# Kernel optimization log

Hardware: AMD Instinct MI355X
Metric: run time of the kernel (lower is better)

The kernel has to match this reference:

```python
import jax, jax.numpy as jnp
import numpy as np
from jax import lax

B, DIM, H, D, P, KER = 256, 1024, 8, 128, 2048, 4  # P = p_factor*DIM, H*D = 1024
HD = H * D

def _lin(key, out_d, in_d):
    return jax.random.normal(key, (out_d, in_d), jnp.float32) * 0.02

def setup_inputs() -> dict:
    key = jax.random.key(0)
    ks = jax.random.split(key, 16)
    return {
        "seq": jax.random.normal(ks[0], (B, DIM), jnp.float32),
        "c_tm1": jnp.zeros((B, H, D, D), jnp.float32),
        "n_tm1": jnp.ones((B, H, D), jnp.float32),
        "m_tm1": jnp.zeros((B, H), jnp.float32),
        "ln_g": jnp.ones((DIM,), jnp.float32), "ln_b": jnp.zeros((DIM,), jnp.float32),
        "Wul": _lin(ks[1], P, DIM), "bul": jnp.zeros((P,), jnp.float32),
        "Wur": _lin(ks[2], HD, DIM), "bur": jnp.zeros((HD,), jnp.float32),
        "conv_w": jax.random.normal(ks[3], (1, 1, KER), jnp.float32) * 0.3,
        "conv_b": jnp.zeros((1,), jnp.float32),
        "Wskip": _lin(ks[4], HD, P),
        "Wi": _lin(ks[5], H, P), "bi": jnp.zeros((H,), jnp.float32),
        "Wf": _lin(ks[6], H, P), "bf": jnp.zeros((H,), jnp.float32),
        "Wo": _lin(ks[7], HD, P), "bo": jnp.zeros((HD,), jnp.float32),
        "Wq": _lin(ks[8], HD, P), "bq": jnp.zeros((HD,), jnp.float32),
        "Wk": _lin(ks[9], HD, P), "bk": jnp.zeros((HD,), jnp.float32),
        "Wv": _lin(ks[10], HD, P), "bv": jnp.zeros((HD,), jnp.float32),
        "gn_g": jnp.ones((HD,), jnp.float32), "gn_b": jnp.zeros((HD,), jnp.float32),
        "Wd": _lin(ks[11], DIM, HD), "bd": jnp.zeros((DIM,), jnp.float32),
    }

def _layernorm(x, g, b, eps=1e-5):
    mu = jnp.mean(x, -1, keepdims=True)
    var = jnp.mean(jnp.square(x - mu), -1, keepdims=True)
    return (x - mu) * lax.rsqrt(var + eps) * g + b

def _groupnorm(x, g, b, h, d, eps=1e-5):
    xh = x.reshape(-1, h, d)
    mu = jnp.mean(xh, -1, keepdims=True)
    var = jnp.mean(jnp.square(xh - mu), -1, keepdims=True)
    xn = (xh - mu) * lax.rsqrt(var + eps)
    return (xn * g.reshape(h, d) + b.reshape(h, d)).reshape(-1, h * d)

def reference(seq, c_tm1, n_tm1, m_tm1, ln_g, ln_b, Wul, bul, Wur, bur, conv_w, conv_b,
              Wskip, Wi, bi, Wf, bf, Wo, bo, Wq, bq, Wk, bk, Wv, bv, gn_g, gn_b, Wd, bd):
    b, h, d = c_tm1.shape[0], c_tm1.shape[1], c_tm1.shape[2]
    ker = conv_w.shape[-1]
    x_n = _layernorm(seq, ln_g, ln_b)
    x_t = x_n @ Wul.T + bul          # [B,P]
    r_t = x_n @ Wur.T + bur          # [B,HD]
    # causal conv along feature axis (Conv1d(1,1,ker) with left pad, trailing pad dropped)
    xp = jnp.pad(x_t[:, None, :], ((0, 0), (0, 0), (ker - 1, 0)))
    x_c = lax.conv_general_dilated(xp, conv_w, (1,), 'VALID')[:, 0, :] + conv_b
    x_c = jax.nn.silu(x_c)           # [B,P]
    q_t = (x_c @ Wq.T + bq).reshape(b, h, d)
    k_t = (x_c @ Wk.T + bk).reshape(b, h, d) / jnp.sqrt(jnp.float32(d))
    v_t = (x_t @ Wv.T + bv).reshape(b, h, d)
    i_t = x_c @ Wi.T + bi            # [B,H]
    f_t = x_c @ Wf.T + bf
    o_t = jax.nn.sigmoid(x_t @ Wo.T + bo)  # [B,HD]
    m_t = jnp.maximum(f_t + m_tm1, i_t)
    i_e = jnp.exp(i_t - m_t)
    f_e = jnp.exp(f_t - m_t + m_tm1)
    c_t = f_e[:, :, None, None] * c_tm1 + i_e[:, :, None, None] * jnp.einsum('bhd,bhp->bhdp', v_t, k_t)
    n_t = f_e[:, :, None] * n_tm1 + i_e[:, :, None] * k_t
    denom = jnp.maximum(jnp.einsum('bhd,bhd->bh', n_t, q_t), 1.0)[:, :, None]
    h_t = o_t * (jnp.einsum('bhdp,bhp->bhd', c_t, q_t) / denom).reshape(b, h * d)
    out = _groupnorm(h_t, gn_g, gn_b, h, d) + x_c @ Wskip.T
    out = out * jax.nn.silu(r_t)
    out = out @ Wd.T + bd
    return out + seq, c_t, n_t, m_t
```

## Files before the change

kernel.cpp:

```cpp
#include <hip/hip_runtime.h>
#include <hip/hip_bf16.h>
#include <math.h>

#define B_   256
#define DIM_ 1024
#define H_   8
#define D_   128
#define P_   2048
#define HD_  1024

typedef short short8 __attribute__((ext_vector_type(8)));
typedef float f32x4 __attribute__((ext_vector_type(4)));

__device__ __forceinline__ float sigf(float x) { return 1.f / (1.f + expf(-x)); }

__device__ __forceinline__ ushort f2bf(float f) {
    return __builtin_bit_cast(unsigned short, __float2bfloat16(f));
}
__device__ __forceinline__ float bf2f(ushort u) {
    unsigned int v = ((unsigned int)u) << 16;
    return __builtin_bit_cast(float, v);
}

#define GLOAD16(gp, lp) \
    __builtin_amdgcn_global_load_lds((const __attribute__((address_space(1))) void*)(gp), \
                                     (__attribute__((address_space(3))) void*)(lp), 16, 0, 0)

#define WOFF_UL    0
#define WOFF_UR    2097152
#define WOFF_Q     3145728
#define WOFF_K     5242880
#define WOFF_SKIP  7340032
#define WOFF_V     9437184
#define WOFF_O     11534336
#define WOFF_D     13631488
#define WOFF_END   14680064

__global__ void wcvt_kernel(const float* __restrict__ s0, const float* __restrict__ s1,
                            const float* __restrict__ s2, const float* __restrict__ s3,
                            const float* __restrict__ s4, const float* __restrict__ s5,
                            const float* __restrict__ s6, const float* __restrict__ s7,
                            ushort* __restrict__ dst) {
    size_t e = ((size_t)blockIdx.x * 256 + threadIdx.x) * 8;
    const float* sp;
    if      (e < WOFF_UR)   { sp = s0 + e; }
    else if (e < WOFF_Q)    { sp = s1 + (e - WOFF_UR); }
    else if (e < WOFF_K)    { sp = s2 + (e - WOFF_Q); }
    else if (e < WOFF_SKIP) { sp = s3 + (e - WOFF_K); }
    else if (e < WOFF_V)    { sp = s4 + (e - WOFF_SKIP); }
    else if (e < WOFF_O)    { sp = s5 + (e - WOFF_V); }
    else if (e < WOFF_D)    { sp = s6 + (e - WOFF_O); }
    else                    { sp = s7 + (e - WOFF_D); }
    f32x4 a = *(const f32x4*)sp;
    f32x4 b = *(const f32x4*)(sp + 4);
    short8 r;
    r[0] = (short)f2bf(a[0]); r[1] = (short)f2bf(a[1]);
    r[2] = (short)f2bf(a[2]); r[3] = (short)f2bf(a[3]);
    r[4] = (short)f2bf(b[0]); r[5] = (short)f2bf(b[1]);
    r[6] = (short)f2bf(b[2]); r[7] = (short)f2bf(b[3]);
    *(short8*)(dst + e) = r;
}

__global__ void ln_kernel(const float* __restrict__ x, const float* __restrict__ g,
                          const float* __restrict__ bt, ushort* __restrict__ y) {
    int b = blockIdx.x, t = threadIdx.x;
    const float* row = x + (size_t)b * DIM_;
    float4 v = *(const float4*)(row + t * 4);
    float s1 = v.x + v.y + v.z + v.w;
    float s2 = v.x * v.x + v.y * v.y + v.z * v.z + v.w * v.w;
    #pragma unroll
    for (int o = 32; o; o >>= 1) { s1 += __shfl_down(s1, o, 64); s2 += __shfl_down(s2, o, 64); }
    __shared__ float r1[4], r2[4];
    __shared__ float mu_s, rs_s;
    int wid = t >> 6, lane = t & 63;
    if (lane == 0) { r1[wid] = s1; r2[wid] = s2; }
    __syncthreads();
    if (t == 0) {
        float S1 = r1[0] + r1[1] + r1[2] + r1[3];
        float S2 = r2[0] + r2[1] + r2[2] + r2[3];
        float mu = S1 / DIM_;
        mu_s = mu;
        rs_s = rsqrtf(S2 / DIM_ - mu * mu + 1e-5f);
    }
    __syncthreads();
    float mu = mu_s, rs = rs_s;
    float4 gg = *(const float4*)(g + t * 4);
    float4 bb = *(const float4*)(bt + t * 4);
    ushort4 o4;
    o4.x = f2bf((v.x - mu) * rs * gg.x + bb.x);
    o4.y = f2bf((v.y - mu) * rs * gg.y + bb.y);
    o4.z = f2bf((v.z - mu) * rs * gg.z + bb.z);
    o4.w = f2bf((v.w - mu) * rs * gg.w + bb.w);
    *(ushort4*)(y + (size_t)b * DIM_ + t * 4) = o4;
}

template <int GID>
__global__ void g_gemm(const ushort* __restrict__ A0, const ushort* __restrict__ A1,
                       const ushort* __restrict__ Wb,
                       const float* __restrict__ b0, const float* __restrict__ b1,
                       const float* __restrict__ b2, const float* __restrict__ b3,
                       const float* __restrict__ b4,
                       float* __restrict__ o0, float* __restrict__ o1, float* __restrict__ o2,
                       float* __restrict__ o3, float* __restrict__ o4v,
                       ushort* __restrict__ aux, const float* __restrict__ seq) {
    constexpr int K = (GID == 1) ? 2048 : 1024;
    constexpr int NT = K / 64;
    const float KSCALE = 0.088388347648318447f;

    __shared__ __align__(16) ushort As[4][64 * 64];
    __shared__ __align__(16) ushort Bs[4][64 * 64];

    int hwid = blockIdx.x;
    int xcd = hwid & 7, q = hwid >> 3;
    int mt = q & 3, g = ((q >> 2) << 3) + xcd;
    int bm = mt << 6, bn = g << 6;

    const ushort* Ab = A0;
    if constexpr (GID == 1) { if (bn >= 3072) Ab = A1; }

    int tid = threadIdx.x;
    int w = tid >> 6, l = tid & 63;
    int wr = w >> 1, wc = w & 1;
    int lr = l & 15, lg = l >> 4;

    int si0 = tid, si1 = 256 + tid;
    int r0 = si0 >> 3, su0 = (si0 & 7) ^ (r0 & 7);
    int r1 = si1 >> 3, su1 = (si1 & 7) ^ (r1 & 7);
    const ushort* gA0 = Ab + (size_t)(bm + r0) * K + su0 * 8;
    const ushort* gA1 = Ab + (size_t)(bm + r1) * K + su1 * 8;
    const ushort* gB0 = Wb + (size_t)(bn + r0) * K + su0 * 8;
    const ushort* gB1 = Wb + (size_t)(bn + r1) * K + su1 * 8;

    f32x4 acc[2][2] = {};

    #pragma unroll
    for (int pt = 0; pt < 2; pt++) {
        int k0 = pt * 64;
        GLOAD16(gA0 + k0, &As[pt][si0 * 8]);
        GLOAD16(gA1 + k0, &As[pt][si1 * 8]);
        GLOAD16(gB0 + k0, &Bs[pt][si0 * 8]);
        GLOAD16(gB1 + k0, &Bs[pt][si1 * 8]);
    }

    for (int t = 0; t < NT; t++) {
        if (t + 2 < NT) {
            int k0 = (t + 2) * 64;
            int nb = (t + 2) & 3;
            GLOAD16(gA0 + k0, &As[nb][si0 * 8]);
            GLOAD16(gA1 + k0, &As[nb][si1 * 8]);
            GLOAD16(gB0 + k0, &Bs[nb][si0 * 8]);
            GLOAD16(gB1 + k0, &Bs[nb][si1 * 8]);
            asm volatile("s_waitcnt vmcnt(8)" ::: "memory");
        } else if (t + 1 < NT) {
            asm volatile("s_waitcnt vmcnt(4)" ::: "memory");
        } else {
            asm volatile("s_waitcnt vmcnt(0)" ::: "memory");
        }
        __builtin_amdgcn_sched_barrier(0);
        __builtin_amdgcn_s_barrier();
        __builtin_amdgcn_sched_barrier(0);

        int cur = t & 3;
        const char* Ac = (const char*)As[cur];
        const char* Bc = (const char*)Bs[cur];
        short8 af[2][2], bf_[2][2];
        #pragma unroll
        for (int mi = 0; mi < 2; mi++) {
            #pragma unroll
            for (int ks = 0; ks < 2; ks++) {
                int r = wr * 32 + mi * 16 + lr;
                int c = (ks * 64 + lg * 16) ^ ((r & 7) << 4);
                af[mi][ks] = *(const short8*)(Ac + r * 128 + c);
            }
        }
        #pragma unroll
        for (int ni = 0; ni < 2; ni++) {
            #pragma unroll
            for (int ks = 0; ks < 2; ks++) {
                int r = wc * 32 + ni * 16 + lr;
                int c = (ks * 64 + lg * 16) ^ ((r & 7) << 4);
                bf_[ni][ks] = *(const short8*)(Bc + r * 128 + c);
            }
        }
        #pragma unroll
        for (int ks = 0; ks < 2; ks++) {
            #pragma unroll
            for (int mi = 0; mi < 2; mi++) {
                #pragma unroll
                for (int ni = 0; ni < 2; ni++) {
                    acc[mi][ni] = __builtin_amdgcn_mfma_f32_16x16x32_bf16(
                        af[mi][ks], bf_[ni][ks], acc[mi][ni], 0, 0, 0);
                }
            }
        }
        __builtin_amdgcn_sched_barrier(0);
    }

    #pragma unroll
    for (int mi = 0; mi < 2; mi++) {
        #pragma unroll
        for (int ni = 0; ni < 2; ni++) {
            int n = bn + wc * 32 + ni * 16 + lr;
            #pragma unroll
            for (int r = 0; r < 4; r++) {
                int m = bm + wr * 32 + mi * 16 + lg * 4 + r;
                float val = acc[mi][ni][r];
                if constexpr (GID == 0) {
                    if (n < 2048) {
                        val += b0[n];
                        o0[(size_t)m * 2048 + n] = val;
                        aux[(size_t)m * 2048 + n] = f2bf(val);
                    } else {
                        int nc = n - 2048;
                        val += b1[nc];
                        o1[(size_t)m * 1024 + nc] = val * sigf(val);
                    }
                } else if constexpr (GID == 1) {
                    if (n < 1024) {
                        o0[(size_t)m * 1024 + n] = val + b0[n];
                    } else if (n < 2048) {
                        int nc = n - 1024;
                        o1[(size_t)m * 1024 + nc] = (val + b1[nc]) * KSCALE;
                    } else if (n < 3072) {
                        int nc = n - 2048;
                        o2[(size_t)m * 1024 + nc] = val;
                    } else if (n < 4096) {
                        int nc = n - 3072;
                        o3[(size_t)m * 1024 + nc] = val + b3[nc];
                    } else {
                        int nc = n - 4096;
                        o4v[(size_t)m * 1024 + nc] = sigf(val + b4[nc]);
                    }
                } else {
                    o0[(size_t)m * 1024 + n] = val + b0[n] + seq[(size_t)m * 1024 + n];
                }
            }
        }
    }
}

__global__ void conv_silu_kernel(const float* __restrict__ x_t, const float* __restrict__ w,
                                 const float* __restrict__ cb, ushort* __restrict__ x_c) {
    int idx = blockIdx.x * 256 + threadIdx.x;
    int b = idx >> 11, p = idx & 2047;
    const float* row = x_t + (size_t)b * P_;
    float acc = cb[0];
    #pragma unroll
    for (int j = 0; j < 4; j++) {
        int pp = p - 3 + j;
        if (pp >= 0) acc = fmaf(w[j], row[pp], acc);
    }
    x_c[idx] = f2bf(acc * (1.f / (1.f + expf(-acc))));
}

__global__ void gates_kernel(const ushort* __restrict__ xc,
                             const float* __restrict__ Wi, const float* __restrict__ Wf,
                             const float* __restrict__ bi, const float* __restrict__ bfp,
                             float* __restrict__ itb, float* __restrict__ ftb) {
    int w = threadIdx.x >> 6, l = threadIdx.x & 63;
    int gid = blockIdx.x * 4 + w;
    int b = gid >> 4, n = gid & 15;
    const float* Wrow = (n < 8) ? (Wi + (size_t)n * 2048) : (Wf + (size_t)(n - 8) * 2048);
    const ushort* arow = xc + (size_t)b * 2048;
    float s = 0.f;
    #pragma unroll
    for (int c = 0; c < 4; c++) {
        int k0 = c * 512 + l * 8;
        short8 a = *(const short8*)(arow + k0);
        f32x4 w0 = *(const f32x4*)(Wrow + k0);
        f32x4 w1 = *(const f32x4*)(Wrow + k0 + 4);
        s = fmaf(bf2f((ushort)a[0]), w0[0], s);
        s = fmaf(bf2f((ushort)a[1]), w0[1], s);
        s = fmaf(bf2f((ushort)a[2]), w0[2], s);
        s = fmaf(bf2f((ushort)a[3]), w0[3], s);
        s = fmaf(bf2f((ushort)a[4]), w1[0], s);
        s = fmaf(bf2f((ushort)a[5]), w1[1], s);
        s = fmaf(bf2f((ushort)a[6]), w1[2], s);
        s = fmaf(bf2f((ushort)a[7]), w1[3], s);
    }
    #pragma unroll
    for (int o = 32; o; o >>= 1) s += __shfl_down(s, o, 64);
    if (l == 0) {
        if (n < 8) itb[b * 8 + n] = s + bi[n];
        else       ftb[b * 8 + (n - 8)] = s + bfp[n - 8];
    }
}

__global__ void cell_kernel(const float* __restrict__ q, const float* __restrict__ k,
                            const float* __restrict__ v, const float* __restrict__ o,
                            const float* __restrict__ i_t, const float* __restrict__ f_t,
                            const float* __restrict__ m_tm1, const float* __restrict__ n_tm1,
                            const float* __restrict__ c_tm1,
                            const float* __restrict__ gn_g, const float* __restrict__ gn_b,
                            const float* __restrict__ skip, const float* __restrict__ sr,
                            float* __restrict__ c_out, float* __restrict__ n_out,
                            float* __restrict__ m_out, ushort* __restrict__ y) {
    int bh = blockIdx.x;
    int h = bh & 7;
    int t = threadIdx.x;
    __shared__ __align__(16) float qs[128];
    __shared__ __align__(16) float ks[128];
    __shared__ __align__(16) float vs[128];
    __shared__ float hnum[128];
    __shared__ float redA[4], redB[4];
    __shared__ float dsh, mu_s, rs_s;

    float fi = i_t[bh], ff = f_t[bh], mo = m_tm1[bh];
    float mt = fmaxf(ff + mo, fi);
    float ie = expf(fi - mt);
    float fe = expf(ff - mt + mo);
    if (t == 0) m_out[bh] = mt;

    int base = bh << 7;
    if (t < 128) { qs[t] = q[base + t]; ks[t] = k[base + t]; vs[t] = v[base + t]; }
    __syncthreads();

    float dn = 0.f;
    if (t < 128) {
        float nt = fe * n_tm1[base + t] + ie * ks[t];
        n_out[base + t] = nt;
        dn = nt * qs[t];
    }
    #pragma unroll
    for (int off2 = 32; off2; off2 >>= 1) dn += __shfl_down(dn, off2, 64);
    int wid = t >> 6, lane = t & 63;
    if (lane == 0) redA[wid] = dn;
    __syncthreads();
    if (t == 0) dsh = fmaxf(redA[0] + redA[1], 1.f);

    const float* cin = c_tm1 + ((size_t)bh << 14);
    float* cout = c_out + ((size_t)bh << 14);
    int l32 = t & 31, grp = t >> 5;
    float4 k4 = *(const float4*)&ks[l32 << 2];
    float4 q4 = *(const float4*)&qs[l32 << 2];
    #pragma unroll
    for (int it2 = 0; it2 < 16; ++it2) {
        int d = (it2 << 3) + grp;
        float vd = vs[d] * ie;
        int off = (d << 7) + (l32 << 2);
        float4 c4 = *(const float4*)(cin + off);
        float4 ct;
        ct.x = fmaf(fe, c4.x, vd * k4.x);
        ct.y = fmaf(fe, c4.y, vd * k4.y);
        ct.z = fmaf(fe, c4.z, vd * k4.z);
        ct.w = fmaf(fe, c4.w, vd * k4.w);
        *(float4*)(cout + off) = ct;
        float p = ct.x * q4.x + ct.y * q4.y + ct.z * q4.z + ct.w * q4.w;
        #pragma unroll
        for (int o2 = 16; o2; o2 >>= 1) p += __shfl_xor(p, o2, 32);
        if (l32 == 0) hnum[d] = p;
    }
    __syncthreads();

    float hval = 0.f;
    if (t < 128) hval = o[base + t] * hnum[t] / dsh;
    float s1 = hval, s2 = hval * hval;
    #pragma unroll
    for (int off2 = 32; off2; off2 >>= 1) { s1 += __shfl_down(s1, off2, 64); s2 += __shfl_down(s2, off2, 64); }
    if (lane == 0) { redA[wid] = s1; redB[wid] = s2; }
    __syncthreads();
    if (t == 0) {
        float S1 = redA[0] + redA[1], S2 = redB[0] + redB[1];
        float mu = S1 / 128.f;
        mu_s = mu;
        rs_s = rsqrtf(S2 / 128.f - mu * mu + 1e-5f);
    }
    __syncthreads();
    if (t < 128) {
        float xn = (hval - mu_s) * rs_s;
        int gi = (h << 7) + t;
        y[base + t] = f2bf((xn * gn_g[gi] + gn_b[gi] + skip[base + t]) * sr[base + t]);
    }
}

extern "C" void kernel_launch(void* const* d_in, const int* in_sizes, int n_in,
                              void* d_out, int out_size, void* d_ws, size_t ws_size,
                              hipStream_t stream) {
    const float* seq    = (const float*)d_in[0];
    const float* c_tm1  = (const float*)d_in[1];
    const float* n_tm1  = (const float*)d_in[2];
    const float* m_tm1  = (const float*)d_in[3];
    const float* ln_g   = (const float*)d_in[4];
    const float* ln_b   = (const float*)d_in[5];
    const float* Wul    = (const float*)d_in[6];
    const float* bul    = (const float*)d_in[7];
    const float* Wur    = (const float*)d_in[8];
    const float* bur    = (const float*)d_in[9];
    const float* conv_w = (const float*)d_in[10];
    const float* conv_b = (const float*)d_in[11];
    const float* Wskip  = (const float*)d_in[12];
    const float* Wi     = (const float*)d_in[13];
    const float* bi     = (const float*)d_in[14];
    const float* Wf     = (const float*)d_in[15];
    const float* bf     = (const float*)d_in[16];
    const float* Wo     = (const float*)d_in[17];
    const float* bo     = (const float*)d_in[18];
    const float* Wq     = (const float*)d_in[19];
    const float* bq     = (const float*)d_in[20];
    const float* Wk     = (const float*)d_in[21];
    const float* bk     = (const float*)d_in[22];
    const float* Wv     = (const float*)d_in[23];
    const float* bv     = (const float*)d_in[24];
    const float* gn_g   = (const float*)d_in[25];
    const float* gn_b   = (const float*)d_in[26];
    const float* Wd     = (const float*)d_in[27];
    const float* bd     = (const float*)d_in[28];

    float* out   = (float*)d_out;
    float* c_out = out + 262144;
    float* n_out = c_out + 33554432;
    float* m_out = n_out + 262144;

    float* ws    = (float*)d_ws;
    float*  x_t  = ws;
    ushort* xnb  = (ushort*)(ws + 524288);
    ushort* xtb  = (ushort*)(ws + 655360);
    float*  sr   = ws + 917504;
    ushort* xcb  = (ushort*)(ws + 1179648);
    float*  qb   = ws + 1441792;
    float*  kb   = ws + 1703936;
    float*  vb   = ws + 1966080;
    float*  ob   = ws + 2228224;
    float*  skipb= ws + 2490368;
    float*  itb  = ws + 2752512;
    float*  ftb  = ws + 2754560;
    ushort* ybf  = (ushort*)(ws + 2756608);
    ushort* wbf  = (ushort*)(ws + 2887680);

    dim3 blk(256);

    wcvt_kernel<<<7168, blk, 0, stream>>>(Wul, Wur, Wq, Wk, Wskip, Wv, Wo, Wd, wbf);
    ln_kernel<<<256, blk, 0, stream>>>(seq, ln_g, ln_b, xnb);
    g_gemm<0><<<192, blk, 0, stream>>>(xnb, nullptr, wbf + WOFF_UL,
                                       bul, bur, nullptr, nullptr, nullptr,
                                       x_t, sr, nullptr, nullptr, nullptr, xtb, nullptr);
    conv_silu_kernel<<<2048, blk, 0, stream>>>(x_t, conv_w, conv_b, xcb);
    gates_kernel<<<1024, blk, 0, stream>>>(xcb, Wi, Wf, bi, bf, itb, ftb);
    g_gemm<1><<<320, blk, 0, stream>>>(xcb, xtb, wbf + WOFF_Q,
                                       bq, bk, nullptr, bv, bo,
                                       qb, kb, skipb, vb, ob, nullptr, nullptr);
    cell_kernel<<<2048, blk, 0, stream>>>(qb, kb, vb, ob, itb, ftb, m_tm1, n_tm1, c_tm1,
                                          gn_g, gn_b, skipb, sr, c_out, n_out, m_out, ybf);
    g_gemm<2><<<64, blk, 0, stream>>>(ybf, nullptr, wbf + WOFF_D,
                                      bd, nullptr, nullptr, nullptr, nullptr,
                                      out, nullptr, nullptr, nullptr, nullptr, nullptr, seq);
}
```

Measured before the change: 388.2 us.

## Fuse layernorm with weight conversion and fold conv and gates into main GEMM

Merges the layernorm and the bf16 weight conversion into one prep kernel. Appends the Wi/Wf gate rows, padded to a tile, to the concatenated weight matrix. The second GEMM now applies the causal conv plus SiLU on the fly from x_t, so the separate conv_silu and gates kernels are gone, along with the xcb buffer and two launches. The trade-off is extra work in the mega GEMM's A-operand path and one additional N-tile column block, 352 blocks instead of 320.

```diff
diff --git a/kernel.cpp b/kernel.cpp
--- a/kernel.cpp
+++ b/kernel.cpp
@@ -2,137 +2,120 @@
 #include <hip/hip_bf16.h>
 #include <math.h>
 
-#define B_   256
-#define DIM_ 1024
-#define H_   8
-#define D_   128
-#define P_   2048
-#define HD_  1024
-
 typedef short short8 __attribute__((ext_vector_type(8)));
 typedef float f32x4 __attribute__((ext_vector_type(4)));
 
 __device__ __forceinline__ float sigf(float x) { return 1.f / (1.f + expf(-x)); }
-
 __device__ __forceinline__ ushort f2bf(float f) {
     return __builtin_bit_cast(unsigned short, __float2bfloat16(f));
 }
-__device__ __forceinline__ float bf2f(ushort u) {
-    unsigned int v = ((unsigned int)u) << 16;
-    return __builtin_bit_cast(float, v);
-}
 
 #define GLOAD16(gp, lp) \
     __builtin_amdgcn_global_load_lds((const __attribute__((address_space(1))) void*)(gp), \
                                      (__attribute__((address_space(3))) void*)(lp), 16, 0, 0)
 
-#define WOFF_UL    0
-#define WOFF_UR    2097152
-#define WOFF_Q     3145728
-#define WOFF_K     5242880
-#define WOFF_SKIP  7340032
-#define WOFF_V     9437184
-#define WOFF_O     11534336
-#define WOFF_D     13631488
-#define WOFF_END   14680064
-
-__global__ void wcvt_kernel(const float* __restrict__ s0, const float* __restrict__ s1,
-                            const float* __restrict__ s2, const float* __restrict__ s3,
-                            const float* __restrict__ s4, const float* __restrict__ s5,
-                            const float* __restrict__ s6, const float* __restrict__ s7,
-                            ushort* __restrict__ dst) {
-    size_t e = ((size_t)blockIdx.x * 256 + threadIdx.x) * 8;
-    const float* sp;
-    if      (e < WOFF_UR)   { sp = s0 + e; }
-    else if (e < WOFF_Q)    { sp = s1 + (e - WOFF_UR); }
-    else if (e < WOFF_K)    { sp = s2 + (e - WOFF_Q); }
-    else if (e < WOFF_SKIP) { sp = s3 + (e - WOFF_K); }
-    else if (e < WOFF_V)    { sp = s4 + (e - WOFF_SKIP); }
-    else if (e < WOFF_O)    { sp = s5 + (e - WOFF_V); }
-    else if (e < WOFF_D)    { sp = s6 + (e - WOFF_O); }
-    else                    { sp = s7 + (e - WOFF_D); }
-    f32x4 a = *(const f32x4*)sp;
-    f32x4 b = *(const f32x4*)(sp + 4);
-    short8 r;
-    r[0] = (short)f2bf(a[0]); r[1] = (short)f2bf(a[1]);
-    r[2] = (short)f2bf(a[2]); r[3] = (short)f2bf(a[3]);
-    r[4] = (short)f2bf(b[0]); r[5] = (short)f2bf(b[1]);
-    r[6] = (short)f2bf(b[2]); r[7] = (short)f2bf(b[3]);
-    *(short8*)(dst + e) = r;
+#define OFF_G0 0
+#define OFF_G1 3145728
+#define OFF_D  14680064
+#define W_END  15728640
+
+__global__ void prep_kernel(const float* __restrict__ seq, const float* __restrict__ ln_g,
+                            const float* __restrict__ ln_b,
+                            const float* __restrict__ Wul, const float* __restrict__ Wur,
+                            const float* __restrict__ Wq, const float* __restrict__ Wk,
+                            const float* __restrict__ Wskip, const float* __restrict__ Wv,
+                            const float* __restrict__ Wo, const float* __restrict__ Wi,
+                            const float* __restrict__ Wf, const float* __restrict__ Wd,
+                            ushort* __restrict__ xnb, ushort* __restrict__ wbf) {
+    int t = threadIdx.x;
+    if (blockIdx.x < 256) {
+        int b = blockIdx.x;
+        const float* row = seq + (size_t)b * 1024;
+        float4 v = *(const float4*)(row + t * 4);
+        float s1 = v.x + v.y + v.z + v.w;
+        float s2 = v.x * v.x + v.y * v.y + v.z * v.z + v.w * v.w;
+        #pragma unroll
+        for (int o = 32; o; o >>= 1) { s1 += __shfl_down(s1, o, 64); s2 += __shfl_down(s2, o, 64); }
+        __shared__ float r1[4], r2[4];
+        __shared__ float mu_s, rs_s;
+        int wid = t >> 6, lane = t & 63;
+        if (lane == 0) { r1[wid] = s1; r2[wid] = s2; }
+        __syncthreads();
+        if (t == 0) {
+            float S1 = r1[0] + r1[1] + r1[2] + r1[3];
+            float S2 = r2[0] + r2[1] + r2[2] + r2[3];
+            float mu = S1 / 1024.f;
+            mu_s = mu;
+            rs_s = rsqrtf(S2 / 1024.f - mu * mu + 1e-5f);
+        }
+        __syncthreads();
+        float mu = mu_s, rs = rs_s;
+        float4 gg = *(const float4*)(ln_g + t * 4);
+        float4 bb = *(const float4*)(ln_b + t * 4);
+        ushort4 o4;
+        o4.x = f2bf((v.x - mu) * rs * gg.x + bb.x);
+        o4.y = f2bf((v.y - mu) * rs * gg.y + bb.y);
+        o4.z = f2bf((v.z - mu) * rs * gg.z + bb.z);
+        o4.w = f2bf((v.w - mu) * rs * gg.w + bb.w);
+        *(ushort4*)(xnb + (size_t)b * 1024 + t * 4) = o4;
+    } else {
+        size_t e = ((size_t)(blockIdx.x - 256) * 256 + t) * 8;
+        const float* sp = nullptr;
+        if (e < OFF_G1) {
+            size_t row = e >> 10, col = e & 1023;
+            sp = (row < 2048 ? Wul + row * 1024 : Wur + (row - 2048) * 1024) + col;
+        } else if (e < OFF_D) {
+            size_t rel = e - OFF_G1;
+            size_t row = rel >> 11, col = rel & 2047;
+            if (row < 1024)      sp = Wq + row * 2048 + col;
+            else if (row < 2048) sp = Wk + (row - 1024) * 2048 + col;
+            else if (row < 3072) sp = Wskip + (row - 2048) * 2048 + col;
+            else if (row < 4096) sp = Wv + (row - 3072) * 2048 + col;
+            else if (row < 5120) sp = Wo + (row - 4096) * 2048 + col;
+            else if (row < 5128) sp = Wi + (row - 5120) * 2048 + col;
+            else if (row < 5136) sp = Wf + (row - 5128) * 2048 + col;
+            else sp = nullptr;
+        } else {
+            sp = Wd + (e - OFF_D);
+        }
+        short8 r;
+        if (sp) {
+            f32x4 a = *(const f32x4*)sp;
+            f32x4 b = *(const f32x4*)(sp + 4);
+            r[0] = (short)f2bf(a[0]); r[1] = (short)f2bf(a[1]);
+            r[2] = (short)f2bf(a[2]); r[3] = (short)f2bf(a[3]);
+            r[4] = (short)f2bf(b[0]); r[5] = (short)f2bf(b[1]);
+            r[6] = (short)f2bf(b[2]); r[7] = (short)f2bf(b[3]);
+        } else {
+            r = (short8){0,0,0,0,0,0,0,0};
+        }
+        *(short8*)(wbf + e) = r;
+    }
 }
 
-__global__ void ln_kernel(const float* __restrict__ x, const float* __restrict__ g,
-                          const float* __restrict__ bt, ushort* __restrict__ y) {
-    int b = blockIdx.x, t = threadIdx.x;
-    const float* row = x + (size_t)b * DIM_;
-    float4 v = *(const float4*)(row + t * 4);
-    float s1 = v.x + v.y + v.z + v.w;
-    float s2 = v.x * v.x + v.y * v.y + v.z * v.z + v.w * v.w;
-    #pragma unroll
-    for (int o = 32; o; o >>= 1) { s1 += __shfl_down(s1, o, 64); s2 += __shfl_down(s2, o, 64); }
-    __shared__ float r1[4], r2[4];
-    __shared__ float mu_s, rs_s;
-    int wid = t >> 6, lane = t & 63;
-    if (lane == 0) { r1[wid] = s1; r2[wid] = s2; }
-    __syncthreads();
-    if (t == 0) {
-        float S1 = r1[0] + r1[1] + r1[2] + r1[3];
-        float S2 = r2[0] + r2[1] + r2[2] + r2[3];
-        float mu = S1 / DIM_;
-        mu_s = mu;
-        rs_s = rsqrtf(S2 / DIM_ - mu * mu + 1e-5f);
-    }
-    __syncthreads();
-    float mu = mu_s, rs = rs_s;
-    float4 gg = *(const float4*)(g + t * 4);
-    float4 bb = *(const float4*)(bt + t * 4);
-    ushort4 o4;
-    o4.x = f2bf((v.x - mu) * rs * gg.x + bb.x);
-    o4.y = f2bf((v.y - mu) * rs * gg.y + bb.y);
-    o4.z = f2bf((v.z - mu) * rs * gg.z + bb.z);
-    o4.w = f2bf((v.w - mu) * rs * gg.w + bb.w);
-    *(ushort4*)(y + (size_t)b * DIM_ + t * 4) = o4;
-}
-
-template <int GID>
-__global__ void g_gemm(const ushort* __restrict__ A0, const ushort* __restrict__ A1,
-                       const ushort* __restrict__ Wb,
-                       const float* __restrict__ b0, const float* __restrict__ b1,
-                       const float* __restrict__ b2, const float* __restrict__ b3,
-                       const float* __restrict__ b4,
-                       float* __restrict__ o0, float* __restrict__ o1, float* __restrict__ o2,
-                       float* __restrict__ o3, float* __restrict__ o4v,
-                       ushort* __restrict__ aux, const float* __restrict__ seq) {
-    constexpr int K = (GID == 1) ? 2048 : 1024;
-    constexpr int NT = K / 64;
-    const float KSCALE = 0.088388347648318447f;
-
-    __shared__ __align__(16) ushort As[4][64 * 64];
-    __shared__ __align__(16) ushort Bs[4][64 * 64];
-
+__global__ void g_gemm0(const ushort* __restrict__ A, const ushort* __restrict__ Wb,
+                        const float* __restrict__ bul, const float* __restrict__ bur,
+                        float* __restrict__ x_t, float* __restrict__ sr,
+                        ushort* __restrict__ xtb) {
+    constexpr int K = 1024, NT = 16;
+    __shared__ __align__(16) ushort As[4][4096];
+    __shared__ __align__(16) ushort Bs[4][4096];
     int hwid = blockIdx.x;
     int xcd = hwid & 7, q = hwid >> 3;
     int mt = q & 3, g = ((q >> 2) << 3) + xcd;
     int bm = mt << 6, bn = g << 6;
-
-    const ushort* Ab = A0;
-    if constexpr (GID == 1) { if (bn >= 3072) Ab = A1; }
-
     int tid = threadIdx.x;
     int w = tid >> 6, l = tid & 63;
     int wr = w >> 1, wc = w & 1;
     int lr = l & 15, lg = l >> 4;
-
     int si0 = tid, si1 = 256 + tid;
     int r0 = si0 >> 3, su0 = (si0 & 7) ^ (r0 & 7);
     int r1 = si1 >> 3, su1 = (si1 & 7) ^ (r1 & 7);
-    const ushort* gA0 = Ab + (size_t)(bm + r0) * K + su0 * 8;
-    const ushort* gA1 = Ab + (size_t)(bm + r1) * K + su1 * 8;
+    const ushort* gA0 = A + (size_t)(bm + r0) * K + su0 * 8;
+    const ushort* gA1 = A + (size_t)(bm + r1) * K + su1 * 8;
     const ushort* gB0 = Wb + (size_t)(bn + r0) * K + su0 * 8;
     const ushort* gB1 = Wb + (size_t)(bn + r1) * K + su1 * 8;
-
     f32x4 acc[2][2] = {};
-
     #pragma unroll
     for (int pt = 0; pt < 2; pt++) {
         int k0 = pt * 64;
@@ -141,11 +124,9 @@
         GLOAD16(gB0 + k0, &Bs[pt][si0 * 8]);
         GLOAD16(gB1 + k0, &Bs[pt][si1 * 8]);
     }
-
     for (int t = 0; t < NT; t++) {
         if (t + 2 < NT) {
-            int k0 = (t + 2) * 64;
-            int nb = (t + 2) & 3;
+            int k0 = (t + 2) * 64, nb = (t + 2) & 3;
             GLOAD16(gA0 + k0, &As[nb][si0 * 8]);
             GLOAD16(gA1 + k0, &As[nb][si1 * 8]);
             GLOAD16(gB0 + k0, &Bs[nb][si0 * 8]);
@@ -159,45 +140,38 @@
         __builtin_amdgcn_sched_barrier(0);
         __builtin_amdgcn_s_barrier();
         __builtin_amdgcn_sched_barrier(0);
-
         int cur = t & 3;
         const char* Ac = (const char*)As[cur];
         const char* Bc = (const char*)Bs[cur];
-        short8 af[2][2], bf_[2][2];
-        #pragma unroll
-        for (int mi = 0; mi < 2; mi++) {
+        short8 af[2][2], bfr[2][2];
+        #pragma unroll
+        for (int mi = 0; mi < 2; mi++)
             #pragma unroll
             for (int ks = 0; ks < 2; ks++) {
                 int r = wr * 32 + mi * 16 + lr;
                 int c = (ks * 64 + lg * 16) ^ ((r & 7) << 4);
                 af[mi][ks] = *(const short8*)(Ac + r * 128 + c);
             }
-        }
-        #pragma unroll
-        for (int ni = 0; ni < 2; ni++) {
+        #pragma unroll
+        for (int ni = 0; ni < 2; ni++)
             #pragma unroll
             for (int ks = 0; ks < 2; ks++) {
                 int r = wc * 32 + ni * 16 + lr;
                 int c = (ks * 64 + lg * 16) ^ ((r & 7) << 4);
-                bf_[ni][ks] = *(const short8*)(Bc + r * 128 + c);
-            }
-        }
-        #pragma unroll
-        for (int ks = 0; ks < 2; ks++) {
-            #pragma unroll
-            for (int mi = 0; mi < 2; mi++) {
-                #pragma unroll
-                for (int ni = 0; ni < 2; ni++) {
+                bfr[ni][ks] = *(const short8*)(Bc + r * 128 + c);
+            }
+        #pragma unroll
+        for (int ks = 0; ks < 2; ks++)
+            #pragma unroll
+            for (int mi = 0; mi < 2; mi++)
+                #pragma unroll
+                for (int ni = 0; ni < 2; ni++)
                     acc[mi][ni] = __builtin_amdgcn_mfma_f32_16x16x32_bf16(
-                        af[mi][ks], bf_[ni][ks], acc[mi][ni], 0, 0, 0);
-                }
-            }
-        }
+                        af[mi][ks], bfr[ni][ks], acc[mi][ni], 0, 0, 0);
         __builtin_amdgcn_sched_barrier(0);
     }
-
-    #pragma unroll
-    for (int mi = 0; mi < 2; mi++) {
+    #pragma unroll
+    for (int mi = 0; mi < 2; mi++)
         #pragma unroll
         for (int ni = 0; ni < 2; ni++) {
             int n = bn + wc * 32 + ni * 16 + lr;
@@ -205,85 +179,224 @@
             for (int r = 0; r < 4; r++) {
                 int m = bm + wr * 32 + mi * 16 + lg * 4 + r;
                 float val = acc[mi][ni][r];
-                if constexpr (GID == 0) {
-                    if (n < 2048) {
-                        val += b0[n];
-                        o0[(size_t)m * 2048 + n] = val;
-                        aux[(size_t)m * 2048 + n] = f2bf(val);
-                    } else {
-                        int nc = n - 2048;
-                        val += b1[nc];
-                        o1[(size_t)m * 1024 + nc] = val * sigf(val);
-                    }
-                } else if constexpr (GID == 1) {
-                    if (n < 1024) {
-                        o0[(size_t)m * 1024 + n] = val + b0[n];
-                    } else if (n < 2048) {
-                        int nc = n - 1024;
-                        o1[(size_t)m * 1024 + nc] = (val + b1[nc]) * KSCALE;
-                    } else if (n < 3072) {
-                        int nc = n - 2048;
-                        o2[(size_t)m * 1024 + nc] = val;
-                    } else if (n < 4096) {
-                        int nc = n - 3072;
-                        o3[(size_t)m * 1024 + nc] = val + b3[nc];
-                    } else {
-                        int nc = n - 4096;
-                        o4v[(size_t)m * 1024 + nc] = sigf(val + b4[nc]);
-                    }
+                if (n < 2048) {
+                    val += bul[n];
+                    x_t[(size_t)m * 2048 + n] = val;
+                    xtb[(size_t)m * 2048 + n] = f2bf(val);
                 } else {
-                    o0[(size_t)m * 1024 + n] = val + b0[n] + seq[(size_t)m * 1024 + n];
+                    int nc = n - 2048;
+                    val += bur[nc];
+                    sr[(size_t)m * 1024 + nc] = val * sigf(val);
                 }
             }
         }
-    }
 }
 
-__global__ void conv_silu_kernel(const float* __restrict__ x_t, const float* __restrict__ w,
-                                 const float* __restrict__ cb, ushort* __restrict__ x_c) {
-    int idx = blockIdx.x * 256 + threadIdx.x;
-    int b = idx >> 11, p = idx & 2047;
-    const float* row = x_t + (size_t)b * P_;
-    float acc = cb[0];
-    #pragma unroll
-    for (int j = 0; j < 4; j++) {
-        int pp = p - 3 + j;
-        if (pp >= 0) acc = fmaf(w[j], row[pp], acc);
-    }
-    x_c[idx] = f2bf(acc * (1.f / (1.f + expf(-acc))));
-}
-
-__global__ void gates_kernel(const ushort* __restrict__ xc,
-                             const float* __restrict__ Wi, const float* __restrict__ Wf,
-                             const float* __restrict__ bi, const float* __restrict__ bfp,
-                             float* __restrict__ itb, float* __restrict__ ftb) {
-    int w = threadIdx.x >> 6, l = threadIdx.x & 63;
-    int gid = blockIdx.x * 4 + w;
-    int b = gid >> 4, n = gid & 15;
-    const float* Wrow = (n < 8) ? (Wi + (size_t)n * 2048) : (Wf + (size_t)(n - 8) * 2048);
-    const ushort* arow = xc + (size_t)b * 2048;
-    float s = 0.f;
-    #pragma unroll
-    for (int c = 0; c < 4; c++) {
-        int k0 = c * 512 + l * 8;
-        short8 a = *(const short8*)(arow + k0);
-        f32x4 w0 = *(const f32x4*)(Wrow + k0);
-        f32x4 w1 = *(const f32x4*)(Wrow + k0 + 4);
-        s = fmaf(bf2f((ushort)a[0]), w0[0], s);
-        s = fmaf(bf2f((ushort)a[1]), w0[1], s);
-        s = fmaf(bf2f((ushort)a[2]), w0[2], s);
-        s = fmaf(bf2f((ushort)a[3]), w0[3], s);
-        s = fmaf(bf2f((ushort)a[4]), w1[0], s);
-        s = fmaf(bf2f((ushort)a[5]), w1[1], s);
-        s = fmaf(bf2f((ushort)a[6]), w1[2], s);
-        s = fmaf(bf2f((ushort)a[7]), w1[3], s);
-    }
-    #pragma unroll
-    for (int o = 32; o; o >>= 1) s += __shfl_down(s, o, 64);
-    if (l == 0) {
-        if (n < 8) itb[b * 8 + n] = s + bi[n];
-        else       ftb[b * 8 + (n - 8)] = s + bfp[n - 8];
-    }
+__global__ void g_mega(const float* __restrict__ xt_f32, const ushort* __restrict__ xtb,
+                       const ushort* __restrict__ Wb,
+                       const float* __restrict__ conv_w, const float* __restrict__ conv_b,
+                       const float* __restrict__ bq, const float* __restrict__ bk,
+                       const float* __restrict__ bv, const float* __restrict__ bo,
+                       const float* __restrict__ bi, const float* __restrict__ bf2,
+                       float* __restrict__ qb, float* __restrict__ kb,
+                       float* __restrict__ skipb, float* __restrict__ vb,
+                       float* __restrict__ ob, float* __restrict__ itb,
+                       float* __restrict__ ftb) {
+    constexpr int K = 2048, NT = 32;
+    const float KSCALE = 0.088388347648318447f;
+    __shared__ __align__(16) ushort As[4][4096];
+    __shared__ __align__(16) ushort Bs[4][4096];
+    int hwid = blockIdx.x;
+    int xcd = hwid & 7, q = hwid >> 3;
+    int mt = q & 3, gq = q >> 2;
+    int g = gq * 8 + xcd;
+    int bm = mt << 6, bn = g << 6;
+    bool is_xc = (bn < 3072) || (bn >= 5120);
+    int tid = threadIdx.x;
+    int w = tid >> 6, l = tid & 63;
+    int wr = w >> 1, wc = w & 1;
+    int lr = l & 15, lg = l >> 4;
+    int si0 = tid, si1 = 256 + tid;
+    int r0 = si0 >> 3, su0 = (si0 & 7) ^ (r0 & 7);
+    int r1 = si1 >> 3, su1 = (si1 & 7) ^ (r1 & 7);
+    const ushort* gB0 = Wb + (size_t)(bn + r0) * K + su0 * 8;
+    const ushort* gB1 = Wb + (size_t)(bn + r1) * K + su1 * 8;
+    f32x4 acc[2][2] = {};
+
+    if (is_xc) {
+        float cw0 = conv_w[0], cw1 = conv_w[1], cw2 = conv_w[2], cw3 = conv_w[3];
+        float cbias = conv_b[0];
+        int ar = tid >> 2, ac4 = tid & 3;
+        const float* arow = xt_f32 + (size_t)(bm + ar) * 2048;
+        int au0 = ((ac4 * 2) ^ (ar & 7)) << 4;
+        int au1 = ((ac4 * 2 + 1) ^ (ar & 7)) << 4;
+        GLOAD16(gB0, &Bs[0][si0 * 8]);
+        GLOAD16(gB1, &Bs[0][si1 * 8]);
+        GLOAD16(gB0 + 64, &Bs[1][si0 * 8]);
+        GLOAD16(gB1 + 64, &Bs[1][si1 * 8]);
+        f32x4 pv0, pv1, pv2, pv3, pv4;
+        {
+            const float* ap = arow + ac4 * 16;
+            if (ac4 == 0) pv0 = (f32x4){0.f, 0.f, 0.f, 0.f};
+            else          pv0 = *(const f32x4*)(ap - 4);
+            pv1 = *(const f32x4*)(ap);
+            pv2 = *(const f32x4*)(ap + 4);
+            pv3 = *(const f32x4*)(ap + 8);
+            pv4 = *(const f32x4*)(ap + 12);
+        }
+        for (int t = 0; t < NT; t++) {
+            f32x4 nv0, nv1, nv2, nv3, nv4;
+            if (t + 1 < NT) {
+                const float* ap = arow + (t + 1) * 64 + ac4 * 16;
+                nv0 = *(const f32x4*)(ap - 4);
+                nv1 = *(const f32x4*)(ap);
+                nv2 = *(const f32x4*)(ap + 4);
+                nv3 = *(const f32x4*)(ap + 8);
+                nv4 = *(const f32x4*)(ap + 12);
+            }
+            if (t + 2 < NT) {
+                int kk = (t + 2) * 64, nb = (t + 2) & 3;
+                GLOAD16(gB0 + kk, &Bs[nb][si0 * 8]);
+                GLOAD16(gB1 + kk, &Bs[nb][si1 * 8]);
+            }
+            float Wv_[20];
+            *(f32x4*)(Wv_ + 0)  = pv0; *(f32x4*)(Wv_ + 4)  = pv1;
+            *(f32x4*)(Wv_ + 8)  = pv2; *(f32x4*)(Wv_ + 12) = pv3;
+            *(f32x4*)(Wv_ + 16) = pv4;
+            short8 p0, p1;
+            #pragma unroll
+            for (int j = 0; j < 16; j++) {
+                float a = fmaf(cw3, Wv_[j + 4], fmaf(cw2, Wv_[j + 3],
+                          fmaf(cw1, Wv_[j + 2], fmaf(cw0, Wv_[j + 1], cbias))));
+                a = a * (1.f / (1.f + expf(-a)));
+                if (j < 8) p0[j] = (short)f2bf(a); else p1[j - 8] = (short)f2bf(a);
+            }
+            char* Aw = (char*)As[t & 1] + ar * 128;
+            *(short8*)(Aw + au0) = p0;
+            *(short8*)(Aw + au1) = p1;
+            asm volatile("s_waitcnt lgkmcnt(0)" ::: "memory");
+            __builtin_amdgcn_sched_barrier(0);
+            __builtin_amdgcn_s_barrier();
+            __builtin_amdgcn_sched_barrier(0);
+            const char* Ac = (const char*)As[t & 1];
+            const char* Bc = (const char*)Bs[t & 3];
+            short8 af[2][2], bfr[2][2];
+            #pragma unroll
+            for (int mi = 0; mi < 2; mi++)
+                #pragma unroll
+                for (int ks = 0; ks < 2; ks++) {
+                    int r = wr * 32 + mi * 16 + lr;
+                    int c = (ks * 64 + lg * 16) ^ ((r & 7) << 4);
+                    af[mi][ks] = *(const short8*)(Ac + r * 128 + c);
+                }
+            #pragma unroll
+            for (int ni = 0; ni < 2; ni++)
+                #pragma unroll
+                for (int ks = 0; ks < 2; ks++) {
+                    int r = wc * 32 + ni * 16 + lr;
+                    int c = (ks * 64 + lg * 16) ^ ((r & 7) << 4);
+                    bfr[ni][ks] = *(const short8*)(Bc + r * 128 + c);
+                }
+            #pragma unroll
+            for (int ks = 0; ks < 2; ks++)
+                #pragma unroll
+                for (int mi = 0; mi < 2; mi++)
+                    #pragma unroll
+                    for (int ni = 0; ni < 2; ni++)
+                        acc[mi][ni] = __builtin_amdgcn_mfma_f32_16x16x32_bf16(
+                            af[mi][ks], bfr[ni][ks], acc[mi][ni], 0, 0, 0);
+            pv0 = nv0; pv1 = nv1; pv2 = nv2; pv3 = nv3; pv4 = nv4;
+            __builtin_amdgcn_sched_barrier(0);
+        }
+    } else {
+        const ushort* gA0 = xtb + (size_t)(bm + r0) * K + su0 * 8;
+        const ushort* gA1 = xtb + (size_t)(bm + r1) * K + su1 * 8;
+        #pragma unroll
+        for (int pt = 0; pt < 2; pt++) {
+            int k0 = pt * 64;
+            GLOAD16(gA0 + k0, &As[pt][si0 * 8]);
+            GLOAD16(gA1 + k0, &As[pt][si1 * 8]);
+            GLOAD16(gB0 + k0, &Bs[pt][si0 * 8]);
+            GLOAD16(gB1 + k0, &Bs[pt][si1 * 8]);
+        }
+        for (int t = 0; t < NT; t++) {
+            if (t + 2 < NT) {
+                int k0 = (t + 2) * 64, nb = (t + 2) & 3;
+                GLOAD16(gA0 + k0, &As[nb][si0 * 8]);
+                GLOAD16(gA1 + k0, &As[nb][si1 * 8]);
+                GLOAD16(gB0 + k0, &Bs[nb][si0 * 8]);
+                GLOAD16(gB1 + k0, &Bs[nb][si1 * 8]);
+                asm volatile("s_waitcnt vmcnt(8)" ::: "memory");
+            } else if (t + 1 < NT) {
+                asm volatile("s_waitcnt vmcnt(4)" ::: "memory");
+            } else {
+                asm volatile("s_waitcnt vmcnt(0)" ::: "memory");
+            }
+            __builtin_amdgcn_sched_barrier(0);
+            __builtin_amdgcn_s_barrier();
+            __builtin_amdgcn_sched_barrier(0);
+            int cur = t & 3;
+            const char* Ac = (const char*)As[cur];
+            const char* Bc = (const char*)Bs[cur];
+            short8 af[2][2], bfr[2][2];
+            #pragma unroll
+            for (int mi = 0; mi < 2; mi++)
+                #pragma unroll
+                for (int ks = 0; ks < 2; ks++) {
+                    int r = wr * 32 + mi * 16 + lr;
+                    int c = (ks * 64 + lg * 16) ^ ((r & 7) << 4);
+                    af[mi][ks] = *(const short8*)(Ac + r * 128 + c);
+                }
+            #pragma unroll
+            for (int ni = 0; ni < 2; ni++)
+                #pragma unroll
+                for (int ks = 0; ks < 2; ks++) {
+                    int r = wc * 32 + ni * 16 + lr;
+                    int c = (ks * 64 + lg * 16) ^ ((r & 7) << 4);
+                    bfr[ni][ks] = *(const short8*)(Bc + r * 128 + c);
+                }
+            #pragma unroll
+            for (int ks = 0; ks < 2; ks++)
+                #pragma unroll
+                for (int mi = 0; mi < 2; mi++)
+                    #pragma unroll
+                    for (int ni = 0; ni < 2; ni++)
+                        acc[mi][ni] = __builtin_amdgcn_mfma_f32_16x16x32_bf16(
+                            af[mi][ks], bfr[ni][ks], acc[mi][ni], 0, 0, 0);
+            __builtin_amdgcn_sched_barrier(0);
+        }
+    }
+
+    int seg = bn >> 10;
+    #pragma unroll
+    for (int mi = 0; mi < 2; mi++)
+        #pragma unroll
+        for (int ni = 0; ni < 2; ni++) {
+            int n = bn + wc * 32 + ni * 16 + lr;
+            #pragma unroll
+            for (int r = 0; r < 4; r++) {
+                int m = bm + wr * 32 + mi * 16 + lg * 4 + r;
+                float val = acc[mi][ni][r];
+                if (seg == 0) {
+                    qb[(size_t)m * 1024 + n] = val + bq[n];
+                } else if (seg == 1) {
+                    int nc = n - 1024;
+                    kb[(size_t)m * 1024 + nc] = (val + bk[nc]) * KSCALE;
+                } else if (seg == 2) {
+                    skipb[(size_t)m * 1024 + (n - 2048)] = val;
+                } else if (seg == 3) {
+                    int nc = n - 3072;
+                    vb[(size_t)m * 1024 + nc] = val + bv[nc];
+                } else if (seg == 4) {
+                    int nc = n - 4096;
+                    ob[(size_t)m * 1024 + nc] = sigf(val + bo[nc]);
+                } else {
+                    int j = n - 5120;
+                    if (j < 8)       itb[m * 8 + j] = val + bi[j];
+                    else if (j < 16) ftb[m * 8 + (j - 8)] = val + bf2[j - 8];
+                }
+            }
+        }
 }
 
 __global__ void cell_kernel(const float* __restrict__ q, const float* __restrict__ k,
@@ -371,6 +484,95 @@
         int gi = (h << 7) + t;
         y[base + t] = f2bf((xn * gn_g[gi] + gn_b[gi] + skip[base + t]) * sr[base + t]);
     }
+}
+
+__global__ void g_gemmD(const ushort* __restrict__ A, const ushort* __restrict__ Wb,
+                        const float* __restrict__ bd, const float* __restrict__ seq,
+                        float* __restrict__ out) {
+    constexpr int K = 1024, NT = 16;
+    __shared__ __align__(16) ushort As[4][4096];
+    __shared__ __align__(16) ushort Bs[4][4096];
+    int hwid = blockIdx.x;
+    int xcd = hwid & 7, q = hwid >> 3;
+    int mt = q & 3, g = ((q >> 2) << 3) + xcd;
+    int bm = mt << 6, bn = g << 6;
+    int tid = threadIdx.x;
+    int w = tid >> 6, l = tid & 63;
+    int wr = w >> 1, wc = w & 1;
+    int lr = l & 15, lg = l >> 4;
+    int si0 = tid, si1 = 256 + tid;
+    int r0 = si0 >> 3, su0 = (si0 & 7) ^ (r0 & 7);
+    int r1 = si1 >> 3, su1 = (si1 & 7) ^ (r1 & 7);
+    const ushort* gA0 = A + (size_t)(bm + r0) * K + su0 * 8;
+    const ushort* gA1 = A + (size_t)(bm + r1) * K + su1 * 8;
+    const ushort* gB0 = Wb + (size_t)(bn + r0) * K + su0 * 8;
+    const ushort* gB1 = Wb + (size_t)(bn + r1) * K + su1 * 8;
+    f32x4 acc[2][2] = {};
+    #pragma unroll
+    for (int pt = 0; pt < 2; pt++) {
+        int k0 = pt * 64;
+        GLOAD16(gA0 + k0, &As[pt][si0 * 8]);
+        GLOAD16(gA1 + k0, &As[pt][si1 * 8]);
+        GLOAD16(gB0 + k0, &Bs[pt][si0 * 8]);
+        GLOAD16(gB1 + k0, &Bs[pt][si1 * 8]);
+    }
+    for (int t = 0; t < NT; t++) {
+        if (t + 2 < NT) {
+            int k0 = (t + 2) * 64, nb = (t + 2) & 3;
+            GLOAD16(gA0 + k0, &As[nb][si0 * 8]);
+            GLOAD16(gA1 + k0, &As[nb][si1 * 8]);
+            GLOAD16(gB0 + k0, &Bs[nb][si0 * 8]);
+            GLOAD16(gB1 + k0, &Bs[nb][si1 * 8]);
+            asm volatile("s_waitcnt vmcnt(8)" ::: "memory");
+        } else if (t + 1 < NT) {
+            asm volatile("s_waitcnt vmcnt(4)" ::: "memory");
+        } else {
+            asm volatile("s_waitcnt vmcnt(0)" ::: "memory");
+        }
+        __builtin_amdgcn_sched_barrier(0);
+        __builtin_amdgcn_s_barrier();
+        __builtin_amdgcn_sched_barrier(0);
+        int cur = t & 3;
+        const char* Ac = (const char*)As[cur];
+        const char* Bc = (const char*)Bs[cur];
+        short8 af[2][2], bfr[2][2];
+        #pragma unroll
+        for (int mi = 0; mi < 2; mi++)
+            #pragma unroll
+            for (int ks = 0; ks < 2; ks++) {
+                int r = wr * 32 + mi * 16 + lr;
+                int c = (ks * 64 + lg * 16) ^ ((r & 7) << 4);
+                af[mi][ks] = *(const short8*)(Ac + r * 128 + c);
+            }
+        #pragma unroll
+        for (int ni = 0; ni < 2; ni++)
+            #pragma unroll
+            for (int ks = 0; ks < 2; ks++) {
+                int r = wc * 32 + ni * 16 + lr;
+                int c = (ks * 64 + lg * 16) ^ ((r & 7) << 4);
+                bfr[ni][ks] = *(const short8*)(Bc + r * 128 + c);
+            }
+        #pragma unroll
+        for (int ks = 0; ks < 2; ks++)
+            #pragma unroll
+            for (int mi = 0; mi < 2; mi++)
+                #pragma unroll
+                for (int ni = 0; ni < 2; ni++)
+                    acc[mi][ni] = __builtin_amdgcn_mfma_f32_16x16x32_bf16(
+                        af[mi][ks], bfr[ni][ks], acc[mi][ni], 0, 0, 0);
+        __builtin_amdgcn_sched_barrier(0);
+    }
+    #pragma unroll
+    for (int mi = 0; mi < 2; mi++)
+        #pragma unroll
+        for (int ni = 0; ni < 2; ni++) {
+            int n = bn + wc * 32 + ni * 16 + lr;
+            #pragma unroll
+            for (int r = 0; r < 4; r++) {
+                int m = bm + wr * 32 + mi * 16 + lg * 4 + r;
+                out[(size_t)m * 1024 + n] = acc[mi][ni][r] + bd[n] + seq[(size_t)m * 1024 + n];
+            }
+        }
 }
 
 extern "C" void kernel_launch(void* const* d_in, const int* in_sizes, int n_in,
@@ -416,32 +618,25 @@
     ushort* xnb  = (ushort*)(ws + 524288);
     ushort* xtb  = (ushort*)(ws + 655360);
     float*  sr   = ws + 917504;
-    ushort* xcb  = (ushort*)(ws + 1179648);
-    float*  qb   = ws + 1441792;
-    float*  kb   = ws + 1703936;
-    float*  vb   = ws + 1966080;
-    float*  ob   = ws + 2228224;
-    float*  skipb= ws + 2490368;
-    float*  itb  = ws + 2752512;
-    float*  ftb  = ws + 2754560;
-    ushort* ybf  = (ushort*)(ws + 2756608);
-    ushort* wbf  = (ushort*)(ws + 2887680);
+    float*  qb   = ws + 1179648;
+    float*  kb   = ws + 1441792;
+    float*  vb   = ws + 1703936;
+    float*  ob   = ws + 1966080;
+    float*  skipb= ws + 2228224;
+    float*  itb  = ws + 2490368;
+    float*  ftb  = ws + 2492416;
+    ushort* ybf  = (ushort*)(ws + 2494464);
+    ushort* wbf  = (ushort*)(ws + 2625536);
 
     dim3 blk(256);
 
-    wcvt_kernel<<<7168, blk, 0, stream>>>(Wul, Wur, Wq, Wk, Wskip, Wv, Wo, Wd, wbf);
-    ln_kernel<<<256, blk, 0, stream>>>(seq, ln_g, ln_b, xnb);
-    g_gemm<0><<<192, blk, 0, stream>>>(xnb, nullptr, wbf + WOFF_UL,
-                                       bul, bur, nullptr, nullptr, nullptr,
-                                       x_t, sr, nullptr, nullptr, nullptr, xtb, nullptr);
-    conv_silu_kernel<<<2048, blk, 0, stream>>>(x_t, conv_w, conv_b, xcb);
-    gates_kernel<<<1024, blk, 0, stream>>>(xcb, Wi, Wf, bi, bf, itb, ftb);
-    g_gemm<1><<<320, blk, 0, stream>>>(xcb, xtb, wbf + WOFF_Q,
-                                       bq, bk, nullptr, bv, bo,
-                                       qb, kb, skipb, vb, ob, nullptr, nullptr);
+    prep_kernel<<<7936, blk, 0, stream>>>(seq, ln_g, ln_b, Wul, Wur, Wq, Wk, Wskip,
+                                          Wv, Wo, Wi, Wf, Wd, xnb, wbf);
+    g_gemm0<<<192, blk, 0, stream>>>(xnb, wbf + OFF_G0, bul, bur, x_t, sr, xtb);
+    g_mega<<<352, blk, 0, stream>>>(x_t, xtb, wbf + OFF_G1, conv_w, conv_b,
+                                    bq, bk, bv, bo, bi, bf,
+                                    qb, kb, skipb, vb, ob, itb, ftb);
     cell_kernel<<<2048, blk, 0, stream>>>(qb, kb, vb, ob, itb, ftb, m_tm1, n_tm1, c_tm1,
                                           gn_g, gn_b, skipb, sr, c_out, n_out, m_out, ybf);
-    g_gemm<2><<<64, blk, 0, stream>>>(ybf, nullptr, wbf + WOFF_D,
-                                      bd, nullptr, nullptr, nullptr, nullptr,
-                                      out, nullptr, nullptr, nullptr, nullptr, nullptr, seq);
+    g_gemmD<<<64, blk, 0, stream>>>(ybf, wbf + OFF_D, bd, seq, out);
 }
```

New measurement: 431.9 us. +11.2%, slower.
